# Kernel tuning notes

Measured on AMD Instinct MI355X. Metric: run time of the kernel, lower is better.

The kernel has to match this reference:

```python
import jax, jax.numpy as jnp
import numpy as np
from jax import lax

KS = 2          # kernel_size (even, so padding=ks/2 makes unfold/fold L match)
PAD = 1         # padding = ks//2
STRIDE = 1      # unfold stride
C_IN = 64
PATCH = KS * KS * C_IN  # 256


def unfold(x, ks, stride, pad):
    # torch.nn.functional.unfold ordering: channel-major, then kernel row, kernel col;
    # L axis is row-major over output positions. Output [B, C*ks*ks, L].
    xp = jnp.pad(x, ((0, 0), (0, 0), (pad, pad), (pad, pad)))
    B, C, H, W = xp.shape
    oh = (H - ks) // stride + 1
    ow = (W - ks) // stride + 1
    pats = jnp.stack(
        [xp[:, :, i:i + stride * oh:stride, j:j + stride * ow:stride]
         for i in range(ks) for j in range(ks)], axis=2)  # [B, C, ks*ks, oh, ow]
    return pats.reshape(B, C * ks * ks, oh * ow)


def fold(cols, Ho, Wo, ks, stride, pad):
    # inverse of unfold: scatter-add patch columns back onto an image.
    B, P, L = cols.shape
    C = P // (ks * ks)
    nb = (Ho + 2 * pad - ks) // stride + 1  # blocks per spatial dim
    cols = cols.reshape(B, C, ks, ks, nb, nb)
    out = jnp.zeros((B, C, Ho + 2 * pad, Wo + 2 * pad), dtype=cols.dtype)
    for ki in range(ks):
        for kj in range(ks):
            out = out.at[:, :, ki:ki + stride * nb:stride,
                         kj:kj + stride * nb:stride].add(cols[:, :, ki, kj])
    return out[:, :, pad:pad + Ho, pad:pad + Wo]


def setup_inputs() -> dict:
    key = jax.random.key(0)
    k1, k2, k3, k4 = jax.random.split(key, 4)
    x = jax.random.normal(k1, (32, C_IN, 56, 56), dtype=jnp.float32)
    weight = jax.random.normal(k2, (128, C_IN, KS, KS), dtype=jnp.float32) * 0.06
    bias = jax.random.normal(k3, (128,), dtype=jnp.float32) * 0.06
    cluster_centers = jax.random.uniform(k4, (512, PATCH), dtype=jnp.float32)
    temp = jnp.float32(1.0)
    return {"x": x, "weight": weight, "bias": bias,
            "cluster_centers": cluster_centers, "temp": temp}


def reference(x, weight, bias, cluster_centers, temp):
    B = x.shape[0]
    cols = unfold(x, KS, STRIDE, PAD)                  # [B, 256, L]
    Bc, P, L = cols.shape
    # faithful to torch: this_patch.view(-1, patch_size) on [B, P, L] (row-major)
    flat = cols.reshape(-1, PATCH)                      # [B*L, 256]
    # Euclidean cdist via gram trick
    x2 = jnp.sum(flat * flat, axis=-1, keepdims=True)   # [N,1]
    c2 = jnp.sum(cluster_centers * cluster_centers, axis=-1)  # [K]
    d = jnp.sqrt(jnp.maximum(x2 + c2 - 2.0 * (flat @ cluster_centers.T), 0.0))
    soft = jax.nn.softmax(-d * temp, axis=1)             # [N, K]
    transformed = soft @ cluster_centers                 # [N, 256]
    final = (temp * transformed + flat) / (temp + 1.0)
    final = final.reshape(Bc, P, L)
    new_size = x.shape[3] * KS                           # 112
    x_refold = fold(final, new_size, new_size, KS, KS, PAD)
    # F.conv2d(x_refold, weight, bias, stride=ks, padding=pad, dilation=groups=1)
    out = lax.conv_general_dilated(
        x_refold, weight, window_strides=(KS, KS),
        padding=[(PAD, PAD), (PAD, PAD)],
        dimension_numbers=("NCHW", "OIHW", "NCHW"))
    return out + bias[None, :, None, None]
```

## Files before the change

### kernel.cpp

```cpp
#include <hip/hip_runtime.h>
#include <hip/hip_bf16.h>
#include <stdint.h>

#define NB    32
#define CIN   64
#define HW    56
#define OHW   57
#define LL    3249
#define PATCH 256
#define NCENT 512
#define OC    128
#define NROWS (NB*LL)
#define NROWS_PAD 104064
#define PL    (PATCH*LL)

typedef __attribute__((ext_vector_type(8))) short short8;
typedef __attribute__((ext_vector_type(4))) float f32x4;
typedef __attribute__((ext_vector_type(4))) int   int4v;
typedef int int4u __attribute__((ext_vector_type(4), aligned(4)));
typedef __attribute__((ext_vector_type(4))) unsigned short ushort4v;
typedef __attribute__((ext_vector_type(8))) unsigned short ushort8;

constexpr size_t OFF_C2   = 0;
constexpr size_t OFF_X2   = 4096;
constexpr size_t OFF_DENP = OFF_X2 + (size_t)NROWS_PAD*4;
constexpr size_t OFF_DEN  = OFF_DENP + (size_t)8*NROWS_PAD*4;
constexpr size_t OFF_CBF  = OFF_DEN + (size_t)NROWS_PAD*4;
constexpr size_t OFF_CTBF = OFF_CBF + (size_t)NCENT*PATCH*2;
constexpr size_t OFF_WBF  = OFF_CTBF + (size_t)PATCH*NCENT*2;
constexpr size_t OFF_FLAT = OFF_WBF + (size_t)OC*PATCH*2;
constexpr size_t OFF_P    = OFF_FLAT + (size_t)NROWS_PAD*PATCH*2;
constexpr size_t OFF_FBM  = OFF_P + (size_t)NROWS_PAD*NCENT*2;

__device__ __forceinline__ unsigned short f2bf(float f) {
    __hip_bfloat16 h = __float2bfloat16(f);
    union { __hip_bfloat16 h; unsigned short u; } v; v.h = h;
    return v.u;
}
__device__ __forceinline__ float bf2f(uint16_t h) {
    union { uint32_t u; float f; } v; v.u = ((uint32_t)h) << 16;
    return v.f;
}
__device__ __forceinline__ void gload16(const void* g, void* l) {
    __builtin_amdgcn_global_load_lds(
        (const __attribute__((address_space(1))) unsigned int*)g,
        (__attribute__((address_space(3))) unsigned int*)l, 16, 0, 0);
}

__global__ __launch_bounds__(256)
void k0a_centers(const float* __restrict__ centers, uint16_t* __restrict__ cbf,
                 uint16_t* __restrict__ ctbf, float* __restrict__ c2) {
    __shared__ float red[4];
    int c = blockIdx.x;
    int k = threadIdx.x;
    float v = centers[c*PATCH + k];
    cbf[c*PATCH + (k ^ ((c & 3) << 3))] = f2bf(v);
    ctbf[k*NCENT + (c ^ ((k & 3) << 3))] = f2bf(v);
    float s = v*v;
    s += __shfl_xor(s, 1);  s += __shfl_xor(s, 2);  s += __shfl_xor(s, 4);
    s += __shfl_xor(s, 8);  s += __shfl_xor(s, 16); s += __shfl_xor(s, 32);
    int w = threadIdx.x >> 6;
    if ((threadIdx.x & 63) == 0) red[w] = s;
    __syncthreads();
    if (threadIdx.x == 0) c2[c] = red[0] + red[1] + red[2] + red[3];
}

__global__ __launch_bounds__(256)
void k0w_weight(const float* __restrict__ weight, uint16_t* __restrict__ wbf) {
    int o = blockIdx.x, p = threadIdx.x;
    wbf[o*PATCH + (p ^ ((o & 3) << 3))] = f2bf(weight[o*PATCH + p]);
}

__global__ __launch_bounds__(256)
void k0b_flat(const float* __restrict__ x, uint16_t* __restrict__ flat,
              float* __restrict__ x2) {
    int tid = threadIdx.x;
    int w = tid >> 6, lane = tid & 63;
    for (int pp = 0; pp < 8; ++pp) {
        int n = blockIdx.x*32 + pp*4 + w;
        int b = n / LL;
        int rr = n - b*LL;
        int k0 = lane*4;
        int o0 = rr*PATCH + k0;
        int p = o0 / LL; int l = o0 - p*LL;
        int i = l / OHW; int j = l - i*OHW;
        float s = 0.f;
        ushort4v pk;
#pragma unroll
        for (int e = 0; e < 4; ++e) {
            float val = 0.f;
            if (n < NROWS) {
                int cc = p >> 2, ki = (p >> 1) & 1, kj = p & 1;
                int y = i + ki - 1, xx = j + kj - 1;
                if ((unsigned)y < HW && (unsigned)xx < HW)
                    val = x[((b*CIN + cc)*HW + y)*HW + xx];
            }
            pk[e] = f2bf(val);
            s += val*val;
            if (++j == OHW) { j = 0; if (++i == OHW) { i = 0; ++p; } }
        }
        *(ushort4v*)(flat + (size_t)n*PATCH + (k0 ^ ((n & 3) << 3))) = pk;
        s += __shfl_xor(s, 1);  s += __shfl_xor(s, 2);  s += __shfl_xor(s, 4);
        s += __shfl_xor(s, 8);  s += __shfl_xor(s, 16); s += __shfl_xor(s, 32);
        if (lane == 0) x2[n] = s;
    }
}

__global__ __launch_bounds__(256, 4)
void k1_scores(const uint16_t* __restrict__ flat, const uint16_t* __restrict__ cbf,
               const float* __restrict__ x2g, const float* __restrict__ c2g,
               const float* __restrict__ temp_p,
               uint16_t* __restrict__ P, float* __restrict__ denp) {
    __shared__ __align__(16) char lds[32768];
    const int tid = threadIdx.x;
    int id = blockIdx.x + 4*blockIdx.y;
    int mt, nt;
    if (id < 3232) { mt = (id & 7) + 8*(id >> 5); nt = (id >> 3) & 3; }
    else { int t = id - 3232; mt = 808 + t % 5; nt = t / 5; }
    const int w = tid >> 6, lane = tid & 63;
    const int wr = w >> 1, wc = w & 1;
    const int l15 = lane & 15, l4 = lane >> 4;

    auto stage = [&](int buf, int kt) {
        const char* srcA = (const char*)flat + (size_t)(mt*128)*512 + kt*64;
        const char* srcB = (const char*)cbf + (size_t)(nt*128)*512 + kt*64;
        char* dA = lds + buf*16384;
        char* dB = dA + 8192;
#pragma unroll
        for (int i = 0; i < 2; ++i) {
            int u = (w*2 + i)*64 + lane;
            int row = u >> 2, sub = u & 3;
            gload16(srcA + (size_t)row*512 + sub*16, dA + u*16);
            gload16(srcB + (size_t)row*512 + sub*16, dB + u*16);
        }
    };

    f32x4 acc[4][4];
#pragma unroll
    for (int i = 0; i < 4; ++i)
#pragma unroll
        for (int j = 0; j < 4; ++j) acc[i][j] = (f32x4)0.f;

    stage(0, 0);
    for (int kt = 0; kt < 8; ++kt) {
        __syncthreads();
        if (kt < 7) stage((kt + 1) & 1, kt + 1);
        const char* A = lds + (kt & 1)*16384;
        const char* B = A + 8192;
        short8 af[4], bfm[4];
#pragma unroll
        for (int rf = 0; rf < 4; ++rf) {
            int row = wr*64 + rf*16 + l15;
            int byte = row*64 + ((l4*16) ^ ((row & 3) << 4));
            af[rf] = *(const short8*)(A + byte);
        }
#pragma unroll
        for (int cf = 0; cf < 4; ++cf) {
            int row = wc*64 + cf*16 + l15;
            int byte = row*64 + ((l4*16) ^ ((row & 3) << 4));
            bfm[cf] = *(const short8*)(B + byte);
        }
#pragma unroll
        for (int rf = 0; rf < 4; ++rf)
#pragma unroll
            for (int cf = 0; cf < 4; ++cf)
                acc[rf][cf] = __builtin_amdgcn_mfma_f32_16x16x32_bf16(
                    af[rf], bfm[cf], acc[rf][cf], 0, 0, 0);
    }

    const float temp = temp_p[0];
    float c2v[4];
#pragma unroll
    for (int cf = 0; cf < 4; ++cf)
        c2v[cf] = c2g[nt*128 + wc*64 + cf*16 + l15];

    float denacc[4][4];
#pragma unroll
    for (int rf = 0; rf < 4; ++rf) {
#pragma unroll
        for (int rr = 0; rr < 4; ++rr) {
            int n = mt*128 + wr*64 + rf*16 + l4*4 + rr;
            float x2v = x2g[n];
            float d = 0.f;
#pragma unroll
            for (int cf = 0; cf < 4; ++cf) {
                float s = x2v + c2v[cf] - 2.f*acc[rf][cf][rr];
                float pv = __expf(-temp * sqrtf(fmaxf(s, 0.f)));
                acc[rf][cf][rr] = pv;
                d += pv;
            }
            denacc[rf][rr] = d;
        }
    }
#pragma unroll
    for (int rf = 0; rf < 4; ++rf)
#pragma unroll
        for (int rr = 0; rr < 4; ++rr) {
            float v = denacc[rf][rr];
            v += __shfl_xor(v, 1); v += __shfl_xor(v, 2);
            v += __shfl_xor(v, 4); v += __shfl_xor(v, 8);
            if (l15 == 0) {
                int n = mt*128 + wr*64 + rf*16 + l4*4 + rr;
                denp[(size_t)(nt*2 + wc)*NROWS_PAD + n] = v;
            }
        }

    __syncthreads();
    uint16_t* Pl = (uint16_t*)lds;
#pragma unroll
    for (int rf = 0; rf < 4; ++rf)
#pragma unroll
        for (int cf = 0; cf < 4; ++cf)
#pragma unroll
            for (int rr = 0; rr < 4; ++rr) {
                int row = wr*64 + rf*16 + l4*4 + rr;
                int cl  = wc*64 + cf*16 + l15;
                Pl[row*128 + (cl ^ ((row & 3) << 3))] = (uint16_t)f2bf(acc[rf][cf][rr]);
            }
    __syncthreads();
#pragma unroll
    for (int i = 0; i < 8; ++i) {
        int c = i*256 + tid;
        int row = c >> 4, sub = c & 15;
        int4v v = *(const int4v*)((const char*)lds + c*16);
        *(int4v*)((char*)P + (size_t)(mt*128 + row)*1024 + nt*256 + sub*16) = v;
    }
}

__global__ __launch_bounds__(128)
void kden(const float* __restrict__ denp, float* __restrict__ den) {
    int n = blockIdx.x*128 + threadIdx.x;
    float s = 0.f;
#pragma unroll
    for (int p = 0; p < 8; ++p) s += denp[(size_t)p*NROWS_PAD + n];
    den[n] = s;
}

__global__ __launch_bounds__(256, 4)
void k2_pv(const uint16_t* __restrict__ P, const uint16_t* __restrict__ ctbf,
           const uint16_t* __restrict__ flat, const float* __restrict__ den,
           const float* __restrict__ temp_p, uint16_t* __restrict__ fbm) {
    __shared__ __align__(16) char lds[32768];
    const int tid = threadIdx.x;
    int id = blockIdx.x + 2*blockIdx.y;
    int mt, nt;
    if (id < 1616) { mt = (id & 7) + 8*(id >> 4); nt = (id >> 3) & 1; }
    else { int t = id - 1616; mt = 808 + t % 5; nt = t / 5; }
    const int w = tid >> 6, lane = tid & 63;
    const int wr = w >> 1, wc = w & 1;
    const int l15 = lane & 15, l4 = lane >> 4;

    auto stage = [&](int buf, int kt) {
        const char* srcA = (const char*)P + (size_t)(mt*128)*1024 + kt*64;
        const char* srcB = (const char*)ctbf + (size_t)(nt*128)*1024 + kt*64;
        char* dA = lds + buf*16384;
        char* dB = dA + 8192;
#pragma unroll
        for (int i = 0; i < 2; ++i) {
            int u = (w*2 + i)*64 + lane;
            int row = u >> 2, sub = u & 3;
            gload16(srcA + (size_t)row*1024 + sub*16, dA + u*16);
            gload16(srcB + (size_t)row*1024 + sub*16, dB + u*16);
        }
    };

    f32x4 acc[4][4];
#pragma unroll
    for (int i = 0; i < 4; ++i)
#pragma unroll
        for (int j = 0; j < 4; ++j) acc[i][j] = (f32x4)0.f;

    stage(0, 0);
    for (int kt = 0; kt < 16; ++kt) {
        __syncthreads();
        if (kt < 15) stage((kt + 1) & 1, kt + 1);
        const char* A = lds + (kt & 1)*16384;
        const char* B = A + 8192;
        short8 af[4], bfm[4];
#pragma unroll
        for (int rf = 0; rf < 4; ++rf) {
            int row = wr*64 + rf*16 + l15;
            int byte = row*64 + ((l4*16) ^ ((row & 3) << 4));
            af[rf] = *(const short8*)(A + byte);
        }
#pragma unroll
        for (int cf = 0; cf < 4; ++cf) {
            int row = wc*64 + cf*16 + l15;
            int byte = row*64 + ((l4*16) ^ ((row & 3) << 4));
            bfm[cf] = *(const short8*)(B + byte);
        }
#pragma unroll
        for (int rf = 0; rf < 4; ++rf)
#pragma unroll
            for (int cf = 0; cf < 4; ++cf)
                acc[rf][cf] = __builtin_amdgcn_mfma_f32_16x16x32_bf16(
                    af[rf], bfm[cf], acc[rf][cf], 0, 0, 0);
    }

    __syncthreads();
    uint16_t* Tl = (uint16_t*)lds;
#pragma unroll
    for (int rf = 0; rf < 4; ++rf)
#pragma unroll
        for (int cf = 0; cf < 4; ++cf)
#pragma unroll
            for (int rr = 0; rr < 4; ++rr) {
                int row = wr*64 + rf*16 + l4*4 + rr;
                int col = wc*64 + cf*16 + l15;
                Tl[row*128 + (col ^ ((row & 7) << 3))] = (uint16_t)f2bf(acc[rf][cf][rr]);
            }
    __syncthreads();

    const float temp = temp_p[0];
    const float inv = 1.f / (temp + 1.f);
#pragma unroll
    for (int i = 0; i < 8; ++i) {
        int ch = i*256 + tid;
        int row = ch >> 4, m0 = (ch & 15)*8;
        int n = mt*128 + row;
        if (n >= NROWS) continue;
        int m = nt*128 + m0;
        float dv = den[n];
        float a1 = temp * inv / dv;
        ushort8 tvv = *(const ushort8*)(Tl + row*128 + (m0 ^ ((row & 7) << 3)));
        ushort8 fl = *(const ushort8*)(flat + (size_t)n*PATCH + (m ^ ((row & 3) << 3)));
        int b = n / LL;
        int rrow = n - b*LL;
        int o = rrow*PATCH + m;
        int p = o / LL; int l = o - p*LL;
        int ii = l / OHW; int jj = l - ii*OHW;
        ushort8 outv;
#pragma unroll
        for (int e = 0; e < 8; ++e) {
            int ki = (p >> 1) & 1, kj = p & 1;
            bool bad = (ii == 0 && ki == 0) || (ii == 56 && ki == 1) ||
                       (jj == 0 && kj == 0) || (jj == 56 && kj == 1);
            float fin = a1*bf2f(tvv[e]) + bf2f(fl[e])*inv;
            outv[e] = bad ? (unsigned short)0 : f2bf(fin);
            if (++jj == OHW) { jj = 0; if (++ii == OHW) { ii = 0; ++p; } }
        }
        *(ushort8*)(fbm + (size_t)n*PATCH + m) = outv;
    }
}

__global__ __launch_bounds__(256, 4)
void k4_conv(const uint16_t* __restrict__ wbf, const uint16_t* __restrict__ fbm,
             const float* __restrict__ bias, float* __restrict__ out) {
    __shared__ __align__(16) char lds[32768];
    const int tid = threadIdx.x;
    const int lt = blockIdx.x;
    const int bb = blockIdx.y;
    const int w = tid >> 6, lane = tid & 63;
    const int wr = w >> 1, wc = w & 1;
    const int l15 = lane & 15, l4 = lane >> 4;

    auto stageA = [&](int buf, int kt) {
        const char* srcA = (const char*)wbf + kt*64;
        char* dA = lds + buf*16384;
#pragma unroll
        for (int i = 0; i < 2; ++i) {
            int u = i*256 + tid;
            int row = u >> 2, sub = u & 3;
            gload16(srcA + (size_t)row*512 + sub*16, dA + u*16);
        }
    };
    auto stageB = [&](int buf, int kt) {
        uint16_t* sB = (uint16_t*)(lds + buf*16384 + 8192);
        int pl = lane & 31;
        int lh = lane >> 5;
#pragma unroll
        for (int i = 0; i < 2; ++i) {
            int l8 = i*8 + w*2 + lh;
            const uint16_t* g = fbm + (size_t)bb*PL + (size_t)(kt*32 + pl)*LL + lt*128 + l8*8;
#pragma unroll
            for (int e = 0; e < 8; ++e) {
                int llocal = l8*8 + e;
                sB[llocal*32 + (pl ^ ((llocal & 3) << 3))] = g[e];
            }
        }
    };

    f32x4 acc[4][4];
#pragma unroll
    for (int i = 0; i < 4; ++i)
#pragma unroll
        for (int j = 0; j < 4; ++j) acc[i][j] = (f32x4)0.f;

    stageA(0, 0); stageB(0, 0);
    for (int kt = 0; kt < 8; ++kt) {
        __syncthreads();
        if (kt < 7) { stageA((kt + 1) & 1, kt + 1); stageB((kt + 1) & 1, kt + 1); }
        const char* A = lds + (kt & 1)*16384;
        const char* B = A + 8192;
        short8 af[4], bfm[4];
#pragma unroll
        for (int rf = 0; rf < 4; ++rf) {
            int row = wr*64 + rf*16 + l15;
            int byte = row*64 + ((l4*16) ^ ((row & 3) << 4));
            af[rf] = *(const short8*)(A + byte);
        }
#pragma unroll
        for (int cf = 0; cf < 4; ++cf) {
            int row = wc*64 + cf*16 + l15;
            int byte = row*64 + ((l4*16) ^ ((row & 3) << 4));
            bfm[cf] = *(const short8*)(B + byte);
        }
#pragma unroll
        for (int rf = 0; rf < 4; ++rf)
#pragma unroll
            for (int cf = 0; cf < 4; ++cf)
                acc[rf][cf] = __builtin_amdgcn_mfma_f32_16x16x32_bf16(
                    af[rf], bfm[cf], acc[rf][cf], 0, 0, 0);
    }

    float bv[4][4];
#pragma unroll
    for (int rf = 0; rf < 4; ++rf)
#pragma unroll
        for (int rr = 0; rr < 4; ++rr)
            bv[rf][rr] = bias[wr*64 + rf*16 + l4*4 + rr];

    float* Ol = (float*)lds;
    for (int half = 0; half < 2; ++half) {
        __syncthreads();
        if (wr == half) {
#pragma unroll
            for (int rf = 0; rf < 4; ++rf)
#pragma unroll
                for (int cf = 0; cf < 4; ++cf)
#pragma unroll
                    for (int rr = 0; rr < 4; ++rr) {
                        int rowl = rf*16 + l4*4 + rr;
                        int col = wc*64 + cf*16 + l15;
                        Ol[rowl*128 + col] = acc[rf][cf][rr] + bv[rf][rr];
                    }
        }
        __syncthreads();
        int base_oc = half*64;
        if (lt < 25) {
#pragma unroll
            for (int i = 0; i < 8; ++i) {
                int c = i*256 + tid;
                int row = c >> 5, sub = c & 31;
                int4u v = *(const int4u*)((const char*)lds + c*16);
                *(int4u*)((char*)out + ((size_t)(bb*OC + base_oc + row)*LL + lt*128 + sub*4)*4) = v;
            }
        } else {
#pragma unroll
            for (int i = 0; i < 8; ++i) {
                int c = i*256 + tid;
                int row = c >> 5, sub = c & 31;
                const float* vp = (const float*)((const char*)lds + c*16);
#pragma unroll
                for (int e = 0; e < 4; ++e) {
                    int l = lt*128 + sub*4 + e;
                    if (l < LL) out[(size_t)(bb*OC + base_oc + row)*LL + l] = vp[e];
                }
            }
        }
    }
}

extern "C" void kernel_launch(void* const* d_in, const int* in_sizes, int n_in,
                              void* d_out, int out_size, void* d_ws, size_t ws_size,
                              hipStream_t stream) {
    const float* x       = (const float*)d_in[0];
    const float* weight  = (const float*)d_in[1];
    const float* bias    = (const float*)d_in[2];
    const float* centers = (const float*)d_in[3];
    const float* temp    = (const float*)d_in[4];
    float* out = (float*)d_out;

    char* ws = (char*)d_ws;
    float*    c2   = (float*)(ws + OFF_C2);
    float*    x2   = (float*)(ws + OFF_X2);
    float*    denp = (float*)(ws + OFF_DENP);
    float*    den  = (float*)(ws + OFF_DEN);
    uint16_t* cbf  = (uint16_t*)(ws + OFF_CBF);
    uint16_t* ctbf = (uint16_t*)(ws + OFF_CTBF);
    uint16_t* wbf  = (uint16_t*)(ws + OFF_WBF);
    uint16_t* flat = (uint16_t*)(ws + OFF_FLAT);
    uint16_t* P    = (uint16_t*)(ws + OFF_P);
    uint16_t* fbm  = (uint16_t*)(ws + OFF_FBM);

    k0a_centers<<<NCENT, 256, 0, stream>>>(centers, cbf, ctbf, c2);
    k0w_weight<<<OC, 256, 0, stream>>>(weight, wbf);
    k0b_flat<<<NROWS_PAD/32, 256, 0, stream>>>(x, flat, x2);
    k1_scores<<<dim3(4, NROWS_PAD/128), 256, 0, stream>>>(flat, cbf, x2, c2, temp, P, denp);
    kden<<<NROWS_PAD/128, 128, 0, stream>>>(denp, den);
    k2_pv<<<dim3(2, NROWS_PAD/128), 256, 0, stream>>>(P, ctbf, flat, den, temp, fbm);
    k4_conv<<<dim3(26, NB), 256, 0, stream>>>(wbf, fbm, bias, out);
}
```

Before: 201.4 us.

## Replace XOR-swizzled tiles with k-chunk-major LDS layout across GEMM kernels

```diff
diff --git a/kernel.cpp b/kernel.cpp
--- a/kernel.cpp
+++ b/kernel.cpp
@@ -54,8 +54,8 @@
     int c = blockIdx.x;
     int k = threadIdx.x;
     float v = centers[c*PATCH + k];
-    cbf[c*PATCH + (k ^ ((c & 3) << 3))] = f2bf(v);
-    ctbf[k*NCENT + (c ^ ((k & 3) << 3))] = f2bf(v);
+    cbf[c*PATCH + k] = f2bf(v);
+    ctbf[k*NCENT + c] = f2bf(v);
     float s = v*v;
     s += __shfl_xor(s, 1);  s += __shfl_xor(s, 2);  s += __shfl_xor(s, 4);
     s += __shfl_xor(s, 8);  s += __shfl_xor(s, 16); s += __shfl_xor(s, 32);
@@ -68,7 +68,7 @@
 __global__ __launch_bounds__(256)
 void k0w_weight(const float* __restrict__ weight, uint16_t* __restrict__ wbf) {
     int o = blockIdx.x, p = threadIdx.x;
-    wbf[o*PATCH + (p ^ ((o & 3) << 3))] = f2bf(weight[o*PATCH + p]);
+    wbf[o*PATCH + p] = f2bf(weight[o*PATCH + p]);
 }
 
 __global__ __launch_bounds__(256)
@@ -99,7 +99,7 @@
             s += val*val;
             if (++j == OHW) { j = 0; if (++i == OHW) { i = 0; ++p; } }
         }
-        *(ushort4v*)(flat + (size_t)n*PATCH + (k0 ^ ((n & 3) << 3))) = pk;
+        *(ushort4v*)(flat + (size_t)n*PATCH + k0) = pk;
         s += __shfl_xor(s, 1);  s += __shfl_xor(s, 2);  s += __shfl_xor(s, 4);
         s += __shfl_xor(s, 8);  s += __shfl_xor(s, 16); s += __shfl_xor(s, 32);
         if (lane == 0) x2[n] = s;
@@ -129,7 +129,7 @@
 #pragma unroll
         for (int i = 0; i < 2; ++i) {
             int u = (w*2 + i)*64 + lane;
-            int row = u >> 2, sub = u & 3;
+            int row = u & 127, sub = u >> 7;
             gload16(srcA + (size_t)row*512 + sub*16, dA + u*16);
             gload16(srcB + (size_t)row*512 + sub*16, dB + u*16);
         }
@@ -151,14 +151,12 @@
 #pragma unroll
         for (int rf = 0; rf < 4; ++rf) {
             int row = wr*64 + rf*16 + l15;
-            int byte = row*64 + ((l4*16) ^ ((row & 3) << 4));
-            af[rf] = *(const short8*)(A + byte);
+            af[rf] = *(const short8*)(A + l4*2048 + row*16);
         }
 #pragma unroll
         for (int cf = 0; cf < 4; ++cf) {
             int row = wc*64 + cf*16 + l15;
-            int byte = row*64 + ((l4*16) ^ ((row & 3) << 4));
-            bfm[cf] = *(const short8*)(B + byte);
+            bfm[cf] = *(const short8*)(B + l4*2048 + row*16);
         }
 #pragma unroll
         for (int rf = 0; rf < 4; ++rf)
@@ -215,7 +213,7 @@
             for (int rr = 0; rr < 4; ++rr) {
                 int row = wr*64 + rf*16 + l4*4 + rr;
                 int cl  = wc*64 + cf*16 + l15;
-                Pl[row*128 + (cl ^ ((row & 3) << 3))] = (uint16_t)f2bf(acc[rf][cf][rr]);
+                Pl[row*128 + cl] = (uint16_t)f2bf(acc[rf][cf][rr]);
             }
     __syncthreads();
 #pragma unroll
@@ -258,7 +256,7 @@
 #pragma unroll
         for (int i = 0; i < 2; ++i) {
             int u = (w*2 + i)*64 + lane;
-            int row = u >> 2, sub = u & 3;
+            int row = u & 127, sub = u >> 7;
             gload16(srcA + (size_t)row*1024 + sub*16, dA + u*16);
             gload16(srcB + (size_t)row*1024 + sub*16, dB + u*16);
         }
@@ -280,14 +278,12 @@
 #pragma unroll
         for (int rf = 0; rf < 4; ++rf) {
             int row = wr*64 + rf*16 + l15;
-            int byte = row*64 + ((l4*16) ^ ((row & 3) << 4));
-            af[rf] = *(const short8*)(A + byte);
+            af[rf] = *(const short8*)(A + l4*2048 + row*16);
         }
 #pragma unroll
         for (int cf = 0; cf < 4; ++cf) {
             int row = wc*64 + cf*16 + l15;
-            int byte = row*64 + ((l4*16) ^ ((row & 3) << 4));
-            bfm[cf] = *(const short8*)(B + byte);
+            bfm[cf] = *(const short8*)(B + l4*2048 + row*16);
         }
 #pragma unroll
         for (int rf = 0; rf < 4; ++rf)
@@ -323,7 +319,7 @@
         float dv = den[n];
         float a1 = temp * inv / dv;
         ushort8 tvv = *(const ushort8*)(Tl + row*128 + (m0 ^ ((row & 7) << 3)));
-        ushort8 fl = *(const ushort8*)(flat + (size_t)n*PATCH + (m ^ ((row & 3) << 3)));
+        ushort8 fl = *(const ushort8*)(flat + (size_t)n*PATCH + m);
         int b = n / LL;
         int rrow = n - b*LL;
         int o = rrow*PATCH + m;
@@ -360,7 +356,7 @@
 #pragma unroll
         for (int i = 0; i < 2; ++i) {
             int u = i*256 + tid;
-            int row = u >> 2, sub = u & 3;
+            int row = u & 127, sub = u >> 7;
             gload16(srcA + (size_t)row*512 + sub*16, dA + u*16);
         }
     };
@@ -396,8 +392,7 @@
 #pragma unroll
         for (int rf = 0; rf < 4; ++rf) {
             int row = wr*64 + rf*16 + l15;
-            int byte = row*64 + ((l4*16) ^ ((row & 3) << 4));
-            af[rf] = *(const short8*)(A + byte);
+            af[rf] = *(const short8*)(A + l4*2048 + row*16);
         }
 #pragma unroll
         for (int cf = 0; cf < 4; ++cf) {
```

After: 257.7 us. +28.0%, slower.
